# Kernel optimization log

Measured on AMD Instinct MI355X. Metric: run time of the kernel, lower is better.

The kernel has to match this reference:

```python
import jax, jax.numpy as jnp
import numpy as np

HEADS = 16
D_HEAD = 64
EPS = 1e-5


def _ln(x, g, b):
    m = jnp.mean(x, axis=-1, keepdims=True)
    v = jnp.var(x, axis=-1, keepdims=True)
    return (x - m) * jax.lax.rsqrt(v + EPS) * g + b


def _attn(xq, xc, Wq, Wk, Wv, Wo, bo):
    # Wq: [dim, inner], Wk/Wv: [ctx_dim, inner], Wo: [inner, dim]
    B, N, _ = xq.shape
    S = xc.shape[1]
    q = (xq @ Wq).reshape(B, N, HEADS, D_HEAD)
    k = (xc @ Wk).reshape(B, S, HEADS, D_HEAD)
    v = (xc @ Wv).reshape(B, S, HEADS, D_HEAD)
    scale = D_HEAD ** -0.5
    scores = jnp.einsum('bnhd,bshd->bhns', q, k) * scale
    attn = jax.nn.softmax(scores, axis=-1)
    out = jnp.einsum('bhns,bshd->bnhd', attn, v).reshape(B, N, HEADS * D_HEAD)
    return out @ Wo + bo


def _geglu_ff(x, Wp, bp, Wf, bf):
    h = x @ Wp + bp  # [B,N,2*inner]
    a, gate = jnp.split(h, 2, axis=-1)
    # torch F.gelu default is exact (erf) gelu
    return (a * jax.nn.gelu(gate, approximate=False)) @ Wf + bf


def setup_inputs() -> dict:
    key = jax.random.key(0)
    ks = jax.random.split(key, 16)
    dim, ctx, inner, ffin = 1024, 768, HEADS * D_HEAD, 4 * 1024
    def w(k, i, o):
        return jax.random.normal(k, (i, o), jnp.float32) * (i ** -0.5)
    inp = {
        'x': jax.random.normal(ks[0], (4, 2048, dim), jnp.float32),
        'context': jax.random.normal(ks[1], (4, 77, ctx), jnp.float32),
        'Wq1': w(ks[2], dim, inner), 'Wk1': w(ks[3], dim, inner), 'Wv1': w(ks[4], dim, inner),
        'Wo1': w(ks[5], inner, dim), 'bo1': jnp.zeros((dim,), jnp.float32),
        'Wq2': w(ks[6], dim, inner), 'Wk2': w(ks[7], ctx, inner), 'Wv2': w(ks[8], ctx, inner),
        'Wo2': w(ks[9], inner, dim), 'bo2': jnp.zeros((dim,), jnp.float32),
        'Wp': w(ks[10], dim, 2 * ffin), 'bp': jnp.zeros((2 * ffin,), jnp.float32),
        'Wf': w(ks[11], ffin, dim), 'bf': jnp.zeros((dim,), jnp.float32),
        'g1': jnp.ones((dim,), jnp.float32), 'b1': jnp.zeros((dim,), jnp.float32),
        'g2': jnp.ones((dim,), jnp.float32), 'b2': jnp.zeros((dim,), jnp.float32),
        'g3': jnp.ones((dim,), jnp.float32), 'b3': jnp.zeros((dim,), jnp.float32),
    }
    return inp


def reference(x, context, Wq1, Wk1, Wv1, Wo1, bo1, Wq2, Wk2, Wv2, Wo2, bo2,
              Wp, bp, Wf, bf, g1, b1, g2, b2, g3, b3):
    x = _attn(_ln(x, g1, b1), _ln(x, g1, b1), Wq1, Wk1, Wv1, Wo1, bo1) + x
    x = _attn(_ln(x, g2, b2), context, Wq2, Wk2, Wv2, Wo2, bo2) + x
    x = _geglu_ff(_ln(x, g3, b3), Wp, bp, Wf, bf) + x
    return x
```

## Files before the change

kernel.cpp:

```cpp
#include <hip/hip_runtime.h>

typedef unsigned short u16;
typedef __bf16 bf16x8 __attribute__((ext_vector_type(8)));
typedef float f32x4 __attribute__((ext_vector_type(4)));

#define HEADS 16
#define DHEAD 64
#define DIM 1024
#define NTOK 2048
#define BATCH 4
#define CTXD 768
#define SCROSS 77
#define FFIN 4096

__device__ inline float bf2f(u16 v) { return __uint_as_float(((unsigned)v) << 16); }
__device__ inline u16 f2bf(float f) {
    unsigned u = __float_as_uint(f);
    unsigned r = u + 0x7fffu + ((u >> 16) & 1u);
    return (u16)(r >> 16);
}
__device__ inline f32x4 f4zero() { f32x4 v; v[0]=0.f; v[1]=0.f; v[2]=0.f; v[3]=0.f; return v; }
__device__ inline bf16x8 as_bf16x8(uint4 u) { union { uint4 a; bf16x8 b; } c; c.a = u; return c.b; }

__device__ inline void gload_lds16(const u16* g, u16* l) {
    __builtin_amdgcn_global_load_lds((const __attribute__((address_space(1))) unsigned*)g,
                                     (__attribute__((address_space(3))) unsigned*)l, 16, 0, 0);
}

__global__ __launch_bounds__(256) void wt_k(const float* __restrict__ W, u16* __restrict__ WT,
                                            int K, int N, float scale, int remap) {
    __shared__ u16 Ts[64][72];
    int k0 = blockIdx.x * 64, n0 = blockIdx.y * 64;
    int t = threadIdx.x;
    int r = t >> 2, c4 = (t & 3) * 16;
    const float* wp = W + (size_t)(k0 + r) * N + n0 + c4;
    #pragma unroll
    for (int j = 0; j < 4; j++) {
        float4 v = *(const float4*)(wp + j * 4);
        Ts[c4 + j * 4 + 0][r] = f2bf(v.x * scale);
        Ts[c4 + j * 4 + 1][r] = f2bf(v.y * scale);
        Ts[c4 + j * 4 + 2][r] = f2bf(v.z * scale);
        Ts[c4 + j * 4 + 3][r] = f2bf(v.w * scale);
    }
    __syncthreads();
    int n = t >> 2, kc = (t & 3) * 16;
    int ng = n0 + n;
    if (remap) ng = ((ng & 4095) >> 4) * 32 + ((ng >> 12) << 4) + (ng & 15);
    u16* op = WT + (size_t)ng * K + k0 + kc;
    *(uint4*)op       = *(const uint4*)&Ts[n][kc];
    *(uint4*)(op + 8) = *(const uint4*)&Ts[n][kc + 8];
}

__global__ __launch_bounds__(256) void cvt_k(const float* __restrict__ X, u16* __restrict__ Y, int n4) {
    int i = blockIdx.x * 256 + threadIdx.x;
    if (i < n4) {
        float4 v = *(const float4*)(X + (size_t)i * 4);
        uint2 o;
        o.x = (unsigned)f2bf(v.x) | ((unsigned)f2bf(v.y) << 16);
        o.y = (unsigned)f2bf(v.z) | ((unsigned)f2bf(v.w) << 16);
        *(uint2*)(Y + (size_t)i * 4) = o;
    }
}

__global__ __launch_bounds__(256) void ln_k(const float* __restrict__ X, const float* __restrict__ G,
                                            const float* __restrict__ Bt, u16* __restrict__ Y) {
    int row = blockIdx.x;
    int t = threadIdx.x;
    int w = t >> 6, lane = t & 63;
    float4 xv = *(const float4*)(X + (size_t)row * DIM + t * 4);
    float s = xv.x + xv.y + xv.z + xv.w;
    float s2 = xv.x*xv.x + xv.y*xv.y + xv.z*xv.z + xv.w*xv.w;
    for (int off = 1; off < 64; off <<= 1) {
        s  += __shfl_xor(s,  off, 64);
        s2 += __shfl_xor(s2, off, 64);
    }
    __shared__ float rs[4], rs2[4];
    if (lane == 0) { rs[w] = s; rs2[w] = s2; }
    __syncthreads();
    float S_ = rs[0] + rs[1] + rs[2] + rs[3];
    float S2_ = rs2[0] + rs2[1] + rs2[2] + rs2[3];
    float mean = S_ * (1.0f / DIM);
    float var = fmaxf(S2_ * (1.0f / DIM) - mean * mean, 0.f);
    float rstd = rsqrtf(var + 1e-5f);
    int col = t * 4;
    float4 g = *(const float4*)(G + col);
    float4 b = *(const float4*)(Bt + col);
    float y0 = (xv.x - mean) * rstd * g.x + b.x;
    float y1 = (xv.y - mean) * rstd * g.y + b.y;
    float y2 = (xv.z - mean) * rstd * g.z + b.z;
    float y3 = (xv.w - mean) * rstd * g.w + b.w;
    uint2 o;
    o.x = (unsigned)f2bf(y0) | ((unsigned)f2bf(y1) << 16);
    o.y = (unsigned)f2bf(y2) | ((unsigned)f2bf(y3) << 16);
    *(uint2*)(Y + (size_t)row * DIM + col) = o;
}

template<typename TC, bool RESID>
__global__ __launch_bounds__(256) void gemm128(const u16* __restrict__ A, int lda,
                                               const u16* __restrict__ BT,
                                               const float* __restrict__ bias, const float* resid,
                                               TC* C, int ldc, int M, int N, int K) {
    __shared__ __align__(16) u16 As[128 * 32];
    __shared__ __align__(16) u16 Bs[128 * 32];
    int m0 = blockIdx.x * 128, n0 = blockIdx.y * 128;
    int t = threadIdx.x;
    int w = t >> 6, lane = t & 63;
    int quad = lane >> 4, l16 = lane & 15;
    int mh = (w & 1) * 64, nh = (w >> 1) * 64;
    f32x4 acc[4][4];
    #pragma unroll
    for (int i = 0; i < 4; i++)
        #pragma unroll
        for (int j = 0; j < 4; j++) acc[i][j] = f4zero();
    int sr = t >> 2;
    int sc8 = (((t & 3) ^ ((sr >> 1) & 3)) * 8);
    int ra0 = min(m0 + sr, M - 1);
    int ra1 = min(m0 + sr + 64, M - 1);
    const u16* ga0 = A + (size_t)ra0 * lda + sc8;
    const u16* ga1 = A + (size_t)ra1 * lda + sc8;
    const u16* gb0 = BT + (size_t)(n0 + sr) * K + sc8;
    const u16* gb1 = BT + (size_t)(n0 + sr + 64) * K + sc8;
    u16* lA0 = &As[w * 512];
    u16* lA1 = &As[2048 + w * 512];
    u16* lB0 = &Bs[w * 512];
    u16* lB1 = &Bs[2048 + w * 512];
    int rq = ((quad ^ ((l16 >> 1) & 3)) * 8);
    for (int k0 = 0; k0 < K; k0 += 32) {
        __syncthreads();
        gload_lds16(ga0 + k0, lA0);
        gload_lds16(ga1 + k0, lA1);
        gload_lds16(gb0 + k0, lB0);
        gload_lds16(gb1 + k0, lB1);
        __syncthreads();
        bf16x8 af[4], bfv[4];
        #pragma unroll
        for (int i = 0; i < 4; i++) {
            af[i]  = as_bf16x8(*(const uint4*)&As[(mh + i * 16 + l16) * 32 + rq]);
            bfv[i] = as_bf16x8(*(const uint4*)&Bs[(nh + i * 16 + l16) * 32 + rq]);
        }
        #pragma unroll
        for (int i = 0; i < 4; i++)
            #pragma unroll
            for (int j = 0; j < 4; j++)
                acc[i][j] = __builtin_amdgcn_mfma_f32_16x16x32_bf16(af[i], bfv[j], acc[i][j], 0, 0, 0);
    }
    #pragma unroll
    for (int j = 0; j < 4; j++) {
        int gn = n0 + nh + j * 16 + l16;
        float bv = bias ? bias[gn] : 0.f;
        #pragma unroll
        for (int i = 0; i < 4; i++) {
            #pragma unroll
            for (int r = 0; r < 4; r++) {
                int gm = m0 + mh + i * 16 + quad * 4 + r;
                if (gm < M) {
                    float v = acc[i][j][r] + bv;
                    if constexpr (RESID) v += resid[(size_t)gm * N + gn];
                    if constexpr (__is_same(TC, u16)) C[(size_t)gm * ldc + gn] = f2bf(v);
                    else                              C[(size_t)gm * ldc + gn] = v;
                }
            }
        }
    }
}


#define BAR() __builtin_amdgcn_s_barrier()
#define SB0() __builtin_amdgcn_sched_barrier(0)
#define PRIO1() __builtin_amdgcn_s_setprio(1)
#define PRIO0() __builtin_amdgcn_s_setprio(0)
#define WAIT_VM6() asm volatile("s_waitcnt vmcnt(6)" ::: "memory")
#define WAIT_VM4() asm volatile("s_waitcnt vmcnt(4)" ::: "memory")
#define WAIT_VM0() asm volatile("s_waitcnt vmcnt(0)" ::: "memory")
#define WAIT_LGKM0() asm volatile("s_waitcnt lgkmcnt(0)" ::: "memory")
#define WAIT_LGKM8() asm volatile("s_waitcnt lgkmcnt(8)" ::: "memory")

#define STAGE_A_R(P, h, q, TAU) gload_lds16(gA + (size_t)((h) * 128 + (q) * 64) * 1024 + (TAU) * 64, \
                                            lA + (P) * 16384 + (h) * 8192 + (q) * 4096)
#define STAGE_B_R(P, h, q, TAU) gload_lds16(gB + (size_t)((h) * 128 + (q) * 64) * 1024 + (TAU) * 64, \
                                            lB + (P) * 16384 + (h) * 8192 + (q) * 4096)
#define RD_A(P, fi, ks) as_bf16x8(*(const uint4*)(rdA + (P) * 32768 + (fi) * 2048 + ((ks) ? o1 : o0)))
#define RD_B(P, fj, ks) as_bf16x8(*(const uint4*)(rdB + (P) * 32768 + (fj) * 2048 + ((ks) ? o1 : o0)))
#define MM(ai, aj, av, bv) acc[ai][aj] = __builtin_amdgcn_mfma_f32_16x16x32_bf16(av, bv, acc[ai][aj], 0, 0, 0)

#define Q00() do { \
    MM(0,0,A0r[0][0],B0r[0][0]); MM(1,0,A0r[1][0],B0r[0][0]); MM(2,0,A0r[2][0],B0r[0][0]); MM(3,0,A0r[3][0],B0r[0][0]); \
    MM(0,1,A0r[0][0],B0r[1][0]); MM(1,1,A0r[1][0],B0r[1][0]); MM(2,1,A0r[2][0],B0r[1][0]); MM(3,1,A0r[3][0],B0r[1][0]); \
    MM(0,0,A0r[0][1],B0r[0][1]); MM(1,0,A0r[1][1],B0r[0][1]); MM(2,0,A0r[2][1],B0r[0][1]); MM(3,0,A0r[3][1],B0r[0][1]); \
    MM(0,1,A0r[0][1],B0r[1][1]); MM(1,1,A0r[1][1],B0r[1][1]); MM(2,1,A0r[2][1],B0r[1][1]); MM(3,1,A0r[3][1],B0r[1][1]); \
} while (0)
#define Q01() do { \
    MM(0,2,A0r[0][0],B1r[0][0]); MM(1,2,A0r[1][0],B1r[0][0]); MM(2,2,A0r[2][0],B1r[0][0]); MM(3,2,A0r[3][0],B1r[0][0]); \
    MM(0,3,A0r[0][0],B1r[1][0]); MM(1,3,A0r[1][0],B1r[1][0]); MM(2,3,A0r[2][0],B1r[1][0]); MM(3,3,A0r[3][0],B1r[1][0]); \
    MM(0,2,A0r[0][1],B1r[0][1]); MM(1,2,A0r[1][1],B1r[0][1]); MM(2,2,A0r[2][1],B1r[0][1]); MM(3,2,A0r[3][1],B1r[0][1]); \
    MM(0,3,A0r[0][1],B1r[1][1]); MM(1,3,A0r[1][1],B1r[1][1]); MM(2,3,A0r[2][1],B1r[1][1]); MM(3,3,A0r[3][1],B1r[1][1]); \
} while (0)
#define Q10() do { \
    MM(4,0,A1r[0][0],B0r[0][0]); MM(5,0,A1r[1][0],B0r[0][0]); MM(6,0,A1r[2][0],B0r[0][0]); MM(7,0,A1r[3][0],B0r[0][0]); \
    MM(4,1,A1r[0][0],B0r[1][0]); MM(5,1,A1r[1][0],B0r[1][0]); MM(6,1,A1r[2][0],B0r[1][0]); MM(7,1,A1r[3][0],B0r[1][0]); \
    MM(4,0,A1r[0][1],B0r[0][1]); MM(5,0,A1r[1][1],B0r[0][1]); MM(6,0,A1r[2][1],B0r[0][1]); MM(7,0,A1r[3][1],B0r[0][1]); \
    MM(4,1,A1r[0][1],B0r[1][1]); MM(5,1,A1r[1][1],B0r[1][1]); MM(6,1,A1r[2][1],B0r[1][1]); MM(7,1,A1r[3][1],B0r[1][1]); \
} while (0)
#define Q11() do { \
    MM(4,2,A1r[0][0],B1r[0][0]); MM(5,2,A1r[1][0],B1r[0][0]); MM(6,2,A1r[2][0],B1r[0][0]); MM(7,2,A1r[3][0],B1r[0][0]); \
    MM(4,3,A1r[0][0],B1r[1][0]); MM(5,3,A1r[1][0],B1r[1][0]); MM(6,3,A1r[2][0],B1r[1][0]); MM(7,3,A1r[3][0],B1r[1][0]); \
    MM(4,2,A1r[0][1],B1r[0][1]); MM(5,2,A1r[1][1],B1r[0][1]); MM(6,2,A1r[2][1],B1r[0][1]); MM(7,2,A1r[3][1],B1r[0][1]); \
    MM(4,3,A1r[0][1],B1r[1][1]); MM(5,3,A1r[1][1],B1r[1][1]); MM(6,3,A1r[2][1],B1r[1][1]); MM(7,3,A1r[3][1],B1r[1][1]); \
} while (0)

#define TILEX(P, S0, S1, T, MIDW, ENDW, LAST) do {                                    \
       \
    B1r[0][0] = RD_B(P, 2, 0); B1r[0][1] = RD_B(P, 2, 1);                             \
    B1r[1][0] = RD_B(P, 3, 0); B1r[1][1] = RD_B(P, 3, 1);                             \
    if (S0) { STAGE_B_R((P) ^ 1, 1, 0, (T) + 1); STAGE_B_R((P) ^ 1, 1, 1, (T) + 1); } \
    SB0(); PRIO1(); Q00(); PRIO0(); SB0();                                            \
                 \
    A1r[0][0] = RD_A(P, 4, 0); A1r[0][1] = RD_A(P, 4, 1);                             \
    A1r[1][0] = RD_A(P, 5, 0); A1r[1][1] = RD_A(P, 5, 1);                             \
    A1r[2][0] = RD_A(P, 6, 0); A1r[2][1] = RD_A(P, 6, 1);                             \
    A1r[3][0] = RD_A(P, 7, 0); A1r[3][1] = RD_A(P, 7, 1);                             \
    if (S1) { STAGE_A_R(P, 0, 0, (T) + 2); STAGE_A_R(P, 1, 0, (T) + 2); }             \
    WAIT_LGKM8(); SB0(); PRIO1(); Q01(); PRIO0(); SB0();                              \
        \
    WAIT_LGKM0();                                                                     \
    if (!(LAST)) { MIDW; BAR(); }                                                     \
    SB0();                                                                            \
                \
    if (!(LAST)) {                                                                    \
        A0r[0][0] = RD_A((P) ^ 1, 0, 0); A0r[0][1] = RD_A((P) ^ 1, 0, 1);             \
        A0r[1][0] = RD_A((P) ^ 1, 1, 0); A0r[1][1] = RD_A((P) ^ 1, 1, 1);             \
        A0r[2][0] = RD_A((P) ^ 1, 2, 0); A0r[2][1] = RD_A((P) ^ 1, 2, 1);             \
        A0r[3][0] = RD_A((P) ^ 1, 3, 0); A0r[3][1] = RD_A((P) ^ 1, 3, 1);             \
    }                                                                                 \
    if (S1) { STAGE_B_R(P, 0, 0, (T) + 2); STAGE_B_R(P, 0, 1, (T) + 2); }             \
    SB0(); PRIO1(); Q10(); PRIO0(); SB0();                                            \
                                \
    if (!(LAST)) {                                                                    \
        B0r[0][0] = RD_B((P) ^ 1, 0, 0); B0r[0][1] = RD_B((P) ^ 1, 0, 1);             \
        B0r[1][0] = RD_B((P) ^ 1, 1, 0); B0r[1][1] = RD_B((P) ^ 1, 1, 1);             \
    }                                                                                 \
       \
    if (S1) { STAGE_A_R(P, 0, 1, (T) + 2); STAGE_A_R(P, 1, 1, (T) + 2); }             \
    SB0(); PRIO1(); Q11(); PRIO0(); SB0();                                            \
    if (!(LAST)) { WAIT_LGKM0(); ENDW; BAR(); }                                       \
    SB0();                                                                            \
} while (0)

template<int NBY, int LDC, int EPI>
__global__ __launch_bounds__(512, 2) void gemm256(const u16* __restrict__ A,
                                                  const u16* __restrict__ BT,
                                                  const float* __restrict__ bias,
                                                  u16* __restrict__ C) {
    __shared__ __align__(16) u16 As[2][16384];
    __shared__ __align__(16) u16 Bs[2][16384];
    int t = threadIdx.x;
    int w = t >> 6, lane = t & 63;
    int quad = lane >> 4, l16 = lane & 15;
    int wm = w >> 2, wn = w & 3;
    int bid = blockIdx.x;
    int cpx = (int)gridDim.x >> 3;
    int swz = (bid & 7) * cpx + (bid >> 3);
    int bx = swz / NBY, by = swz % NBY;
    int m0 = bx << 8, n0 = by << 8;

    int ar = t >> 3;
    int ac = (((t & 7) ^ (ar & 7)) << 3);
    const u16* gA = A + (size_t)(m0 + ar) * 1024 + ac;
    const u16* gB = BT + (size_t)(n0 + ar) * 1024 + ac;
    u16* lA = &As[0][0] + (w << 9);
    u16* lB = &Bs[0][0] + (w << 9);
    const char* rdA = (const char*)&As[0][0] + (((wm << 7) + l16) << 7);
    const char* rdB = (const char*)&Bs[0][0] + (((wn << 6) + l16) << 7);
    int o0 = (quad << 4) ^ ((l16 & 7) << 4);
    int o1 = o0 ^ 64;

    f32x4 acc[8][4];
    #pragma unroll
    for (int i = 0; i < 8; i++)
        #pragma unroll
        for (int j = 0; j < 4; j++) acc[i][j] = f4zero();

    STAGE_A_R(0, 0, 0, 0); STAGE_A_R(0, 1, 0, 0);
    STAGE_B_R(0, 0, 0, 0); STAGE_B_R(0, 0, 1, 0);
    STAGE_A_R(0, 0, 1, 0); STAGE_A_R(0, 1, 1, 0);
    STAGE_B_R(0, 1, 0, 0); STAGE_B_R(0, 1, 1, 0);
    STAGE_A_R(1, 0, 0, 1); STAGE_A_R(1, 1, 0, 1);
    STAGE_B_R(1, 0, 0, 1); STAGE_B_R(1, 0, 1, 1);
    STAGE_A_R(1, 0, 1, 1); STAGE_A_R(1, 1, 1, 1);
    WAIT_VM6();
    BAR();
    bf16x8 A0r[4][2], A1r[4][2], B0r[2][2], B1r[2][2];
    A0r[0][0] = RD_A(0, 0, 0); A0r[0][1] = RD_A(0, 0, 1);
    A0r[1][0] = RD_A(0, 1, 0); A0r[1][1] = RD_A(0, 1, 1);
    A0r[2][0] = RD_A(0, 2, 0); A0r[2][1] = RD_A(0, 2, 1);
    A0r[3][0] = RD_A(0, 3, 0); A0r[3][1] = RD_A(0, 3, 1);
    B0r[0][0] = RD_B(0, 0, 0); B0r[0][1] = RD_B(0, 0, 1);
    B0r[1][0] = RD_B(0, 1, 0); B0r[1][1] = RD_B(0, 1, 1);
    WAIT_LGKM0();
    BAR();

    #pragma unroll 1
    for (int tt = 0; tt < 14; tt += 2) {
        TILEX(0, 1, 1, tt,     WAIT_VM6(), WAIT_VM6(), 0);
        TILEX(1, 1, 1, tt + 1, WAIT_VM6(), WAIT_VM6(), 0);
    }
    TILEX(0, 1, 0, 14, WAIT_VM4(), WAIT_VM0(), 0);
    TILEX(1, 0, 0, 15, (void)0, (void)0, 1);

    if constexpr (EPI == 0) {
        int gm0 = m0 + wm * 128 + quad * 4;
        int gn0 = n0 + wn * 64 + l16;
        #pragma unroll
        for (int fi = 0; fi < 8; fi++)
            #pragma unroll
            for (int fj = 0; fj < 4; fj++)
                #pragma unroll
                for (int r = 0; r < 4; r++)
                    C[(size_t)(gm0 + fi * 16 + r) * LDC + gn0 + fj * 16] = f2bf(acc[fi][fj][r]);
    } else {
        int gm0 = m0 + wm * 128 + quad * 4;
        int oc0 = (n0 >> 1) + wn * 32 + l16;
        #pragma unroll
        for (int jp = 0; jp < 2; jp++) {
            int oc = oc0 + jp * 16;
            float ba = bias[oc];
            float bg = bias[FFIN + oc];
            #pragma unroll
            for (int fi = 0; fi < 8; fi++)
                #pragma unroll
                for (int r = 0; r < 4; r++) {
                    float a = acc[fi][2 * jp][r] + ba;
                    float g = acc[fi][2 * jp + 1][r] + bg;
                    float v = a * (0.5f * g * (1.f + erff(g * 0.70710678118654752f)));
                    C[(size_t)(gm0 + fi * 16 + r) * LDC + oc] = f2bf(v);
                }
        }
    }
}

__global__ __launch_bounds__(256) void attn_k(const u16* Q, int ldq, const u16* __restrict__ K,
                                              const u16* __restrict__ V, int ldkv,
                                              u16* O, int S) {
    __shared__ __align__(16) u16 Ksh[128 * 64];
    __shared__ __align__(16) u16 Vt[64 * 128];
    __shared__ __align__(16) u16 Pb[4][16 * 128];
    int bh = blockIdx.x;
    int b = bh >> 4, h = bh & 15;
    int q0 = blockIdx.y * 64;
    int t = threadIdx.x;
    int w = t >> 6, lane = t & 63;
    int quad = lane >> 4, l16 = lane & 15;
    int sw = (l16 & 7) << 3;
    const u16* Qp = Q + ((size_t)b * NTOK + q0) * ldq + h * DHEAD;
    const u16* Kp = K + (size_t)b * S * ldkv + h * DHEAD;
    const u16* Vp = V + (size_t)b * S * ldkv + h * DHEAD;
    bf16x8 qf[2];
    #pragma unroll
    for (int ds = 0; ds < 2; ds++)
        qf[ds] = as_bf16x8(*(const uint4*)(Qp + (size_t)(w * 16 + l16) * ldq + ds * 32 + quad * 8));
    float l_l = 0.f;
    f32x4 o_acc[4];
    #pragma unroll
    for (int dt = 0; dt < 4; dt++) o_acc[dt] = f4zero();
    int kr8 = lane >> 3;
    int ksl = ((lane & 7) ^ kr8) * 8;
    int vd = (t >> 5) * 8;
    int vk = (t & 31) * 4;
    int nkt = (S + 127) / 128;
    union V4 { uint4 u; u16 e[8]; };
    V4 vrC[4], vrN[4];
    #pragma unroll
    for (int j = 0; j < 4; j++) {
        int key = min(vk + j, S - 1);
        vrC[j].u = *(const uint4*)(Vp + (size_t)key * ldkv + vd);
    }
    for (int kt = 0; kt < nkt; kt++) {
        int kbase = kt * 128;
        bool full = (kbase + 128) <= S;
        __syncthreads();
        #pragma unroll
        for (int i = 0; i < 4; i++) {
            int r = min(kbase + (i * 4 + w) * 8 + kr8, S - 1);
            gload_lds16(Kp + (size_t)r * ldkv + ksl, &Ksh[(i * 4 + w) * 512]);
        }
        #pragma unroll
        for (int d = 0; d < 8; d++) {
            int row = vd + d;
            uint2 p;
            p.x = (unsigned)vrC[0].e[d] | ((unsigned)vrC[1].e[d] << 16);
            p.y = (unsigned)vrC[2].e[d] | ((unsigned)vrC[3].e[d] << 16);
            *(uint2*)&Vt[row * 128 + (vk ^ ((row & 7) << 3))] = p;
        }
        __syncthreads();
        f32x4 sc[8];
        PRIO1();
        #pragma unroll
        for (int sub = 0; sub < 8; sub++) {
            const u16* kr = &Ksh[(sub * 16 + l16) * 64];
            bf16x8 kf0 = as_bf16x8(*(const uint4*)(kr + ((quad * 8) ^ sw)));
            bf16x8 kf1 = as_bf16x8(*(const uint4*)(kr + ((32 + quad * 8) ^ sw)));
            f32x4 s = __builtin_amdgcn_mfma_f32_16x16x32_bf16(kf0, qf[0], f4zero(), 0, 0, 0);
            sc[sub] = __builtin_amdgcn_mfma_f32_16x16x32_bf16(kf1, qf[1], s, 0, 0, 0);
        }
        PRIO0();
        if (kt + 1 < nkt) {
            #pragma unroll
            for (int j = 0; j < 4; j++) {
                int key = min(kbase + 128 + vk + j, S - 1);
                vrN[j].u = *(const uint4*)(Vp + (size_t)key * ldkv + vd);
            }
        }
        if (!full) {
            #pragma unroll
            for (int sub = 0; sub < 8; sub++)
                #pragma unroll
                for (int r = 0; r < 4; r++)
                    if (kbase + sub * 16 + quad * 4 + r >= S) sc[sub][r] = -1e30f;
        }
        float psum = 0.f;
        #pragma unroll
        for (int sub = 0; sub < 8; sub++) {
            float p0 = __builtin_amdgcn_exp2f(sc[sub][0]);
            float p1 = __builtin_amdgcn_exp2f(sc[sub][1]);
            float p2 = __builtin_amdgcn_exp2f(sc[sub][2]);
            float p3 = __builtin_amdgcn_exp2f(sc[sub][3]);
            psum += (p0 + p1) + (p2 + p3);
            uint2 pk;
            pk.x = __builtin_amdgcn_perm(__float_as_uint(p1), __float_as_uint(p0), 0x07060302);
            pk.y = __builtin_amdgcn_perm(__float_as_uint(p3), __float_as_uint(p2), 0x07060302);
            *(uint2*)&Pb[w][l16 * 128 + ((sub * 16 + quad * 4) ^ sw)] = pk;
        }
        l_l += psum;
        PRIO1();
        #pragma unroll
        for (int kk = 0; kk < 4; kk++) {
            bf16x8 pf = as_bf16x8(*(const uint4*)&Pb[w][l16 * 128 + ((kk * 32 + quad * 8) ^ sw)]);
            #pragma unroll
            for (int dt = 0; dt < 4; dt++) {
                bf16x8 vf = as_bf16x8(*(const uint4*)&Vt[(dt * 16 + l16) * 128 + ((kk * 32 + quad * 8) ^ sw)]);
                o_acc[dt] = __builtin_amdgcn_mfma_f32_16x16x32_bf16(pf, vf, o_acc[dt], 0, 0, 0);
            }
        }
        PRIO0();
        #pragma unroll
        for (int j = 0; j < 4; j++) vrC[j] = vrN[j];
    }
    float l_tot = l_l;
    l_tot += __shfl_xor(l_tot, 16, 64);
    l_tot += __shfl_xor(l_tot, 32, 64);
    #pragma unroll
    for (int r = 0; r < 4; r++) {
        float lr = __shfl(l_tot, quad * 4 + r, 64);
        float invl = (lr > 0.f) ? (1.f / lr) : 0.f;
        int gq = q0 + w * 16 + quad * 4 + r;
        #pragma unroll
        for (int dt = 0; dt < 4; dt++) {
            O[((size_t)b * NTOK + gq) * ldq + h * DHEAD + dt * 16 + l16] = f2bf(o_acc[dt][r] * invl);
        }
    }
}

extern "C" void kernel_launch(void* const* d_in, const int* in_sizes, int n_in,
                              void* d_out, int out_size, void* d_ws, size_t ws_size,
                              hipStream_t stream) {
    const float* x   = (const float*)d_in[0];
    const float* ctx = (const float*)d_in[1];
    const float* Wq1 = (const float*)d_in[2];
    const float* Wk1 = (const float*)d_in[3];
    const float* Wv1 = (const float*)d_in[4];
    const float* Wo1 = (const float*)d_in[5];
    const float* bo1 = (const float*)d_in[6];
    const float* Wq2 = (const float*)d_in[7];
    const float* Wk2 = (const float*)d_in[8];
    const float* Wv2 = (const float*)d_in[9];
    const float* Wo2 = (const float*)d_in[10];
    const float* bo2 = (const float*)d_in[11];
    const float* Wp  = (const float*)d_in[12];
    const float* bp  = (const float*)d_in[13];
    const float* Wf  = (const float*)d_in[14];
    const float* bfb = (const float*)d_in[15];
    const float* g1  = (const float*)d_in[16];
    const float* b1  = (const float*)d_in[17];
    const float* g2  = (const float*)d_in[18];
    const float* b2  = (const float*)d_in[19];
    const float* g3  = (const float*)d_in[20];
    const float* b3  = (const float*)d_in[21];
    float* out = (float*)d_out;

    const int M = BATCH * NTOK;
    const int Mc = BATCH * SCROSS;
    u16* ws = (u16*)d_ws;
    size_t o = 0;
    u16* WqT1 = ws + o; o += (size_t)DIM * DIM;
    u16* WkT1 = ws + o; o += (size_t)DIM * DIM;
    u16* WvT1 = ws + o; o += (size_t)DIM * DIM;
    u16* WoT1 = ws + o; o += (size_t)DIM * DIM;
    u16* WqT2 = ws + o; o += (size_t)DIM * DIM;
    u16* WoT2 = ws + o; o += (size_t)DIM * DIM;
    u16* WkT2 = ws + o; o += (size_t)DIM * CTXD;
    u16* WvT2 = ws + o; o += (size_t)DIM * CTXD;
    u16* WpT  = ws + o; o += (size_t)(2 * FFIN) * DIM;
    u16* WfT  = ws + o; o += (size_t)DIM * FFIN;
    u16* ctxb = ws + o; o += (size_t)Mc * CTXD;
    u16* KVc  = ws + o; o += (size_t)Mc * 2048;
    u16* P    = ws + o; o += (size_t)M * DIM;
    u16* QKV  = ws + o; o += (size_t)M * 3072;
    u16* reg2 = ws + o; o += (size_t)M * DIM * 2;
    float* X1 = (float*)reg2;
    u16* gb = QKV;

    dim3 blk(256);
    const float qscale = 0.125f * 1.4426950408889634f;

    wt_k<<<dim3(16, 16), blk, 0, stream>>>(Wq1, WqT1, DIM, DIM, qscale, 0);
    wt_k<<<dim3(16, 16), blk, 0, stream>>>(Wk1, WkT1, DIM, DIM, 1.f, 0);
    wt_k<<<dim3(16, 16), blk, 0, stream>>>(Wv1, WvT1, DIM, DIM, 1.f, 0);
    wt_k<<<dim3(16, 16), blk, 0, stream>>>(Wo1, WoT1, DIM, DIM, 1.f, 0);
    wt_k<<<dim3(16, 16), blk, 0, stream>>>(Wq2, WqT2, DIM, DIM, qscale, 0);
    wt_k<<<dim3(16, 16), blk, 0, stream>>>(Wo2, WoT2, DIM, DIM, 1.f, 0);
    wt_k<<<dim3(12, 16), blk, 0, stream>>>(Wk2, WkT2, CTXD, DIM, 1.f, 0);
    wt_k<<<dim3(12, 16), blk, 0, stream>>>(Wv2, WvT2, CTXD, DIM, 1.f, 0);
    wt_k<<<dim3(16, 128), blk, 0, stream>>>(Wp, WpT, DIM, 2 * FFIN, 1.f, 1);
    wt_k<<<dim3(64, 16), blk, 0, stream>>>(Wf, WfT, FFIN, DIM, 1.f, 0);
    cvt_k<<<dim3((Mc * CTXD / 4 + 255) / 256), blk, 0, stream>>>(ctx, ctxb, Mc * CTXD / 4);

    ln_k<<<dim3(M), blk, 0, stream>>>(x, g1, b1, P);
    gemm256<12, 3072, 0><<<dim3(32 * 12), dim3(512), 0, stream>>>(P, WqT1, nullptr, QKV);
    attn_k<<<dim3(BATCH * HEADS, NTOK / 64), blk, 0, stream>>>(
        QKV, 3072, QKV + 1024, QKV + 2048, 3072, QKV, NTOK);
    gemm128<float, true><<<dim3(M / 128, DIM / 128), blk, 0, stream>>>(
        QKV, 3072, WoT1, bo1, x, X1, DIM, M, DIM, DIM);

    ln_k<<<dim3(M), blk, 0, stream>>>(X1, g2, b2, P);
    gemm128<u16, false><<<dim3(M / 128, DIM / 128), blk, 0, stream>>>(
        P, DIM, WqT2, nullptr, nullptr, QKV, 3072, M, DIM, DIM);
    gemm128<u16, false><<<dim3((Mc + 127) / 128, 2048 / 128), blk, 0, stream>>>(
        ctxb, CTXD, WkT2, nullptr, nullptr, KVc, 2048, Mc, 2048, CTXD);
    attn_k<<<dim3(BATCH * HEADS, NTOK / 64), blk, 0, stream>>>(
        QKV, 3072, KVc, KVc + 1024, 2048, QKV, SCROSS);
    gemm128<float, true><<<dim3(M / 128, DIM / 128), blk, 0, stream>>>(
        QKV, 3072, WoT2, bo2, X1, out, DIM, M, DIM, DIM);

    ln_k<<<dim3(M), blk, 0, stream>>>(out, g3, b3, P);
    gemm_geglu_dispatch:
    gemm256<32, 4096, 1><<<dim3(32 * 32), dim3(512), 0, stream>>>(P, WpT, bp, gb);
    gemm128<float, true><<<dim3(M / 128, DIM / 128), blk, 0, stream>>>(
        gb, FFIN, WfT, bfb, out, out, DIM, M, DIM, FFIN);
}
```

Measured before the change: 863.3 us.

## Process 128 queries per attention block to reuse K/V tiles across two fragments

The attention kernel now handles 128 query rows per block, with each wave owning two 16-row query fragments instead of one. Each K and V tile staged in shared memory now feeds twice as many MFMAs, which halves K/V global loads and LDS staging per query and halves the grid size. The cost is more registers for accumulators and Q fragments, a doubled P buffer in LDS, and fewer blocks in flight, which may lower occupancy. The softmax still skips max subtraction, as before.

```diff
diff --git a/kernel.cpp b/kernel.cpp
--- a/kernel.cpp
+++ b/kernel.cpp
@@ -209,23 +209,19 @@
 } while (0)
 
 #define TILEX(P, S0, S1, T, MIDW, ENDW, LAST) do {                                    \
-       \
     B1r[0][0] = RD_B(P, 2, 0); B1r[0][1] = RD_B(P, 2, 1);                             \
     B1r[1][0] = RD_B(P, 3, 0); B1r[1][1] = RD_B(P, 3, 1);                             \
     if (S0) { STAGE_B_R((P) ^ 1, 1, 0, (T) + 1); STAGE_B_R((P) ^ 1, 1, 1, (T) + 1); } \
     SB0(); PRIO1(); Q00(); PRIO0(); SB0();                                            \
-                 \
     A1r[0][0] = RD_A(P, 4, 0); A1r[0][1] = RD_A(P, 4, 1);                             \
     A1r[1][0] = RD_A(P, 5, 0); A1r[1][1] = RD_A(P, 5, 1);                             \
     A1r[2][0] = RD_A(P, 6, 0); A1r[2][1] = RD_A(P, 6, 1);                             \
     A1r[3][0] = RD_A(P, 7, 0); A1r[3][1] = RD_A(P, 7, 1);                             \
     if (S1) { STAGE_A_R(P, 0, 0, (T) + 2); STAGE_A_R(P, 1, 0, (T) + 2); }             \
     WAIT_LGKM8(); SB0(); PRIO1(); Q01(); PRIO0(); SB0();                              \
-        \
     WAIT_LGKM0();                                                                     \
     if (!(LAST)) { MIDW; BAR(); }                                                     \
     SB0();                                                                            \
-                \
     if (!(LAST)) {                                                                    \
         A0r[0][0] = RD_A((P) ^ 1, 0, 0); A0r[0][1] = RD_A((P) ^ 1, 0, 1);             \
         A0r[1][0] = RD_A((P) ^ 1, 1, 0); A0r[1][1] = RD_A((P) ^ 1, 1, 1);             \
@@ -234,12 +230,10 @@
     }                                                                                 \
     if (S1) { STAGE_B_R(P, 0, 0, (T) + 2); STAGE_B_R(P, 0, 1, (T) + 2); }             \
     SB0(); PRIO1(); Q10(); PRIO0(); SB0();                                            \
-                                \
     if (!(LAST)) {                                                                    \
         B0r[0][0] = RD_B((P) ^ 1, 0, 0); B0r[0][1] = RD_B((P) ^ 1, 0, 1);             \
         B0r[1][0] = RD_B((P) ^ 1, 1, 0); B0r[1][1] = RD_B((P) ^ 1, 1, 1);             \
     }                                                                                 \
-       \
     if (S1) { STAGE_A_R(P, 0, 1, (T) + 2); STAGE_A_R(P, 1, 1, (T) + 2); }             \
     SB0(); PRIO1(); Q11(); PRIO0(); SB0();                                            \
     if (!(LAST)) { WAIT_LGKM0(); ENDW; BAR(); }                                       \
@@ -343,10 +337,10 @@
                                               u16* O, int S) {
     __shared__ __align__(16) u16 Ksh[128 * 64];
     __shared__ __align__(16) u16 Vt[64 * 128];
-    __shared__ __align__(16) u16 Pb[4][16 * 128];
+    __shared__ __align__(16) u16 Pb[4][32 * 128];
     int bh = blockIdx.x;
     int b = bh >> 4, h = bh & 15;
-    int q0 = blockIdx.y * 64;
+    int q0 = blockIdx.y * 128;
     int t = threadIdx.x;
     int w = t >> 6, lane = t & 63;
     int quad = lane >> 4, l16 = lane & 15;
@@ -354,14 +348,18 @@
     const u16* Qp = Q + ((size_t)b * NTOK + q0) * ldq + h * DHEAD;
     const u16* Kp = K + (size_t)b * S * ldkv + h * DHEAD;
     const u16* Vp = V + (size_t)b * S * ldkv + h * DHEAD;
-    bf16x8 qf[2];
-    #pragma unroll
-    for (int ds = 0; ds < 2; ds++)
-        qf[ds] = as_bf16x8(*(const uint4*)(Qp + (size_t)(w * 16 + l16) * ldq + ds * 32 + quad * 8));
-    float l_l = 0.f;
-    f32x4 o_acc[4];
-    #pragma unroll
-    for (int dt = 0; dt < 4; dt++) o_acc[dt] = f4zero();
+    bf16x8 qf[2][2];
+    #pragma unroll
+    for (int f = 0; f < 2; f++)
+        #pragma unroll
+        for (int ds = 0; ds < 2; ds++)
+            qf[f][ds] = as_bf16x8(*(const uint4*)(Qp + (size_t)(w * 32 + f * 16 + l16) * ldq + ds * 32 + quad * 8));
+    float l_l[2] = {0.f, 0.f};
+    f32x4 o_acc[2][4];
+    #pragma unroll
+    for (int f = 0; f < 2; f++)
+        #pragma unroll
+        for (int dt = 0; dt < 4; dt++) o_acc[f][dt] = f4zero();
     int kr8 = lane >> 3;
     int ksl = ((lane & 7) ^ kr8) * 8;
     int vd = (t >> 5) * 8;
@@ -392,70 +390,78 @@
             *(uint2*)&Vt[row * 128 + (vk ^ ((row & 7) << 3))] = p;
         }
         __syncthreads();
-        f32x4 sc[8];
+        #pragma unroll
+        for (int f = 0; f < 2; f++) {
+            f32x4 sc[8];
+            PRIO1();
+            #pragma unroll
+            for (int sub = 0; sub < 8; sub++) {
+                const u16* kr = &Ksh[(sub * 16 + l16) * 64];
+                bf16x8 kf0 = as_bf16x8(*(const uint4*)(kr + ((quad * 8) ^ sw)));
+                bf16x8 kf1 = as_bf16x8(*(const uint4*)(kr + ((32 + quad * 8) ^ sw)));
+                f32x4 s = __builtin_amdgcn_mfma_f32_16x16x32_bf16(kf0, qf[f][0], f4zero(), 0, 0, 0);
+                sc[sub] = __builtin_amdgcn_mfma_f32_16x16x32_bf16(kf1, qf[f][1], s, 0, 0, 0);
+            }
+            PRIO0();
+            if (f == 0 && kt + 1 < nkt) {
+                #pragma unroll
+                for (int j = 0; j < 4; j++) {
+                    int key = min(kbase + 128 + vk + j, S - 1);
+                    vrN[j].u = *(const uint4*)(Vp + (size_t)key * ldkv + vd);
+                }
+            }
+            if (!full) {
+                #pragma unroll
+                for (int sub = 0; sub < 8; sub++)
+                    #pragma unroll
+                    for (int r = 0; r < 4; r++)
+                        if (kbase + sub * 16 + quad * 4 + r >= S) sc[sub][r] = -1e30f;
+            }
+            float psum = 0.f;
+            #pragma unroll
+            for (int sub = 0; sub < 8; sub++) {
+                float p0 = __builtin_amdgcn_exp2f(sc[sub][0]);
+                float p1 = __builtin_amdgcn_exp2f(sc[sub][1]);
+                float p2 = __builtin_amdgcn_exp2f(sc[sub][2]);
+                float p3 = __builtin_amdgcn_exp2f(sc[sub][3]);
+                psum += (p0 + p1) + (p2 + p3);
+                uint2 pk;
+                pk.x = __builtin_amdgcn_perm(__float_as_uint(p1), __float_as_uint(p0), 0x07060302);
+                pk.y = __builtin_amdgcn_perm(__float_as_uint(p3), __float_as_uint(p2), 0x07060302);
+                *(uint2*)&Pb[w][(f * 16 + l16) * 128 + ((sub * 16 + quad * 4) ^ sw)] = pk;
+            }
+            l_l[f] += psum;
+        }
         PRIO1();
         #pragma unroll
-        for (int sub = 0; sub < 8; sub++) {
-            const u16* kr = &Ksh[(sub * 16 + l16) * 64];
-            bf16x8 kf0 = as_bf16x8(*(const uint4*)(kr + ((quad * 8) ^ sw)));
-            bf16x8 kf1 = as_bf16x8(*(const uint4*)(kr + ((32 + quad * 8) ^ sw)));
-            f32x4 s = __builtin_amdgcn_mfma_f32_16x16x32_bf16(kf0, qf[0], f4zero(), 0, 0, 0);
-            sc[sub] = __builtin_amdgcn_mfma_f32_16x16x32_bf16(kf1, qf[1], s, 0, 0, 0);
-        }
-        PRIO0();
-        if (kt + 1 < nkt) {
-            #pragma unroll
-            for (int j = 0; j < 4; j++) {
-                int key = min(kbase + 128 + vk + j, S - 1);
-                vrN[j].u = *(const uint4*)(Vp + (size_t)key * ldkv + vd);
-            }
-        }
-        if (!full) {
-            #pragma unroll
-            for (int sub = 0; sub < 8; sub++)
-                #pragma unroll
-                for (int r = 0; r < 4; r++)
-                    if (kbase + sub * 16 + quad * 4 + r >= S) sc[sub][r] = -1e30f;
-        }
-        float psum = 0.f;
-        #pragma unroll
-        for (int sub = 0; sub < 8; sub++) {
-            float p0 = __builtin_amdgcn_exp2f(sc[sub][0]);
-            float p1 = __builtin_amdgcn_exp2f(sc[sub][1]);
-            float p2 = __builtin_amdgcn_exp2f(sc[sub][2]);
-            float p3 = __builtin_amdgcn_exp2f(sc[sub][3]);
-            psum += (p0 + p1) + (p2 + p3);
-            uint2 pk;
-            pk.x = __builtin_amdgcn_perm(__float_as_uint(p1), __float_as_uint(p0), 0x07060302);
-            pk.y = __builtin_amdgcn_perm(__float_as_uint(p3), __float_as_uint(p2), 0x07060302);
-            *(uint2*)&Pb[w][l16 * 128 + ((sub * 16 + quad * 4) ^ sw)] = pk;
-        }
-        l_l += psum;
-        PRIO1();
-        #pragma unroll
         for (int kk = 0; kk < 4; kk++) {
-            bf16x8 pf = as_bf16x8(*(const uint4*)&Pb[w][l16 * 128 + ((kk * 32 + quad * 8) ^ sw)]);
+            bf16x8 pf0 = as_bf16x8(*(const uint4*)&Pb[w][(l16) * 128 + ((kk * 32 + quad * 8) ^ sw)]);
+            bf16x8 pf1 = as_bf16x8(*(const uint4*)&Pb[w][(16 + l16) * 128 + ((kk * 32 + quad * 8) ^ sw)]);
             #pragma unroll
             for (int dt = 0; dt < 4; dt++) {
                 bf16x8 vf = as_bf16x8(*(const uint4*)&Vt[(dt * 16 + l16) * 128 + ((kk * 32 + quad * 8) ^ sw)]);
-                o_acc[dt] = __builtin_amdgcn_mfma_f32_16x16x32_bf16(pf, vf, o_acc[dt], 0, 0, 0);
+                o_acc[0][dt] = __builtin_amdgcn_mfma_f32_16x16x32_bf16(pf0, vf, o_acc[0][dt], 0, 0, 0);
+                o_acc[1][dt] = __builtin_amdgcn_mfma_f32_16x16x32_bf16(pf1, vf, o_acc[1][dt], 0, 0, 0);
             }
         }
         PRIO0();
         #pragma unroll
         for (int j = 0; j < 4; j++) vrC[j] = vrN[j];
     }
-    float l_tot = l_l;
-    l_tot += __shfl_xor(l_tot, 16, 64);
-    l_tot += __shfl_xor(l_tot, 32, 64);
-    #pragma unroll
-    for (int r = 0; r < 4; r++) {
-        float lr = __shfl(l_tot, quad * 4 + r, 64);
-        float invl = (lr > 0.f) ? (1.f / lr) : 0.f;
-        int gq = q0 + w * 16 + quad * 4 + r;
-        #pragma unroll
-        for (int dt = 0; dt < 4; dt++) {
-            O[((size_t)b * NTOK + gq) * ldq + h * DHEAD + dt * 16 + l16] = f2bf(o_acc[dt][r] * invl);
+    #pragma unroll
+    for (int f = 0; f < 2; f++) {
+        float l_tot = l_l[f];
+        l_tot += __shfl_xor(l_tot, 16, 64);
+        l_tot += __shfl_xor(l_tot, 32, 64);
+        #pragma unroll
+        for (int r = 0; r < 4; r++) {
+            float lr = __shfl(l_tot, quad * 4 + r, 64);
+            float invl = (lr > 0.f) ? (1.f / lr) : 0.f;
+            int gq = q0 + w * 32 + f * 16 + quad * 4 + r;
+            #pragma unroll
+            for (int dt = 0; dt < 4; dt++) {
+                O[((size_t)b * NTOK + gq) * ldq + h * DHEAD + dt * 16 + l16] = f2bf(o_acc[f][dt][r] * invl);
+            }
         }
     }
 }
@@ -526,7 +532,7 @@
 
     ln_k<<<dim3(M), blk, 0, stream>>>(x, g1, b1, P);
     gemm256<12, 3072, 0><<<dim3(32 * 12), dim3(512), 0, stream>>>(P, WqT1, nullptr, QKV);
-    attn_k<<<dim3(BATCH * HEADS, NTOK / 64), blk, 0, stream>>>(
+    attn_k<<<dim3(BATCH * HEADS, NTOK / 128), blk, 0, stream>>>(
         QKV, 3072, QKV + 1024, QKV + 2048, 3072, QKV, NTOK);
     gemm128<float, true><<<dim3(M / 128, DIM / 128), blk, 0, stream>>>(
         QKV, 3072, WoT1, bo1, x, X1, DIM, M, DIM, DIM);
@@ -536,13 +542,12 @@
         P, DIM, WqT2, nullptr, nullptr, QKV, 3072, M, DIM, DIM);
     gemm128<u16, false><<<dim3((Mc + 127) / 128, 2048 / 128), blk, 0, stream>>>(
         ctxb, CTXD, WkT2, nullptr, nullptr, KVc, 2048, Mc, 2048, CTXD);
-    attn_k<<<dim3(BATCH * HEADS, NTOK / 64), blk, 0, stream>>>(
+    attn_k<<<dim3(BATCH * HEADS, NTOK / 128), blk, 0, stream>>>(
         QKV, 3072, KVc, KVc + 1024, 2048, QKV, SCROSS);
     gemm128<float, true><<<dim3(M / 128, DIM / 128), blk, 0, stream>>>(
         QKV, 3072, WoT2, bo2, X1, out, DIM, M, DIM, DIM);
 
     ln_k<<<dim3(M), blk, 0, stream>>>(out, g3, b3, P);
-    gemm_geglu_dispatch:
     gemm256<32, 4096, 1><<<dim3(32 * 32), dim3(512), 0, stream>>>(P, WpT, bp, gb);
     gemm128<float, true><<<dim3(M / 128, DIM / 128), blk, 0, stream>>>(
         gb, FFIN, WfT, bfb, out, out, DIM, M, DIM, FFIN);
```

Result: no change. 862.7 us (-0.1%).
